# Kernel tuning notes

Hardware: AMD Instinct MI355X
Metric: run time of the kernel (lower is better)

## Reference

```python
import jax, jax.numpy as jnp
import numpy as np

PAD, BOS, EOS, ROW, SEP = 10, 11, 12, 13, 14
VOCAB, D_MODEL, MAX_SEQ, MAX_H, MAX_W = 15, 512, 4096, 30, 30
B, T = 16, 4096
LN_EPS = 1e-5


def _build_2d_ids(ids):
    """Replicates the serial CPU double-loop as a vectorized lax.scan over time.
    ids: (B, T) int32 -> (row_ids, col_ids), each (B, T) int32."""
    def step(carry, tok):
        row, col, in_grid = carry
        is_bos = tok == BOS
        is_sep = tok == SEP
        is_row = tok == ROW
        is_end = (tok == EOS) | (tok == PAD)
        grid_color = in_grid & (tok >= 0) & (tok <= 9)
        emit_r = jnp.where(grid_color, row, 0)
        emit_c = jnp.where(grid_color, col, 0)
        n_grid = jnp.where(is_bos, True, jnp.where(is_end, False, in_grid))
        n_row = jnp.where(is_bos | is_sep, 0, jnp.where(is_row, row + 1, row))
        n_col = jnp.where(is_bos | is_sep | is_row, 0,
                          jnp.where(grid_color, col + 1, col))
        return (n_row, n_col, n_grid), (emit_r, emit_c)

    def scan_one(seq):
        init = (jnp.int32(0), jnp.int32(0), jnp.bool_(False))
        _, (r, c) = jax.lax.scan(step, init, seq)
        return r, c

    r, c = jax.vmap(scan_one)(ids)
    return jnp.clip(r, 0, MAX_H - 1), jnp.clip(c, 0, MAX_W - 1)


def setup_inputs() -> dict:
    key = jax.random.key(0)
    ks = jax.random.split(key, 8)
    input_ids = jax.random.randint(ks[0], (B, T), 0, VOCAB, dtype=jnp.int32)
    s = 0.02
    token_table = jax.random.normal(ks[1], (VOCAB, D_MODEL), jnp.float32) * s
    token_table = token_table.at[PAD].set(0.0)  # padding_idx zeroed
    pos_table = jax.random.normal(ks[2], (MAX_SEQ, D_MODEL), jnp.float32) * s
    row_table = jax.random.normal(ks[3], (MAX_H, D_MODEL // 2), jnp.float32) * s
    col_table = jax.random.normal(ks[4], (MAX_W, D_MODEL // 2), jnp.float32) * s
    w_spatial = jax.random.normal(ks[5], (D_MODEL, D_MODEL), jnp.float32) * s
    ln_gamma = jnp.ones((D_MODEL,), jnp.float32)
    ln_beta = jnp.zeros((D_MODEL,), jnp.float32)
    return {"input_ids": input_ids, "token_table": token_table,
            "pos_table": pos_table, "row_table": row_table,
            "col_table": col_table, "w_spatial": w_spatial,
            "ln_gamma": ln_gamma, "ln_beta": ln_beta}


def reference(input_ids, token_table, pos_table, row_table, col_table,
              w_spatial, ln_gamma, ln_beta):
    Bv, Tv = input_ids.shape
    tok_emb = token_table[input_ids]                      # (B,T,D)
    pos_emb = pos_table[:Tv][None, :, :]                  # (1,T,D)
    row_ids, col_ids = _build_2d_ids(input_ids)
    rc = jnp.concatenate([row_table[row_ids], col_table[col_ids]], axis=-1)
    spatial = jnp.einsum('btd,ed->bte', rc, w_spatial)    # Linear, no bias
    mask = ((input_ids >= 0) & (input_ids <= 9)).astype(tok_emb.dtype)[..., None]
    x = tok_emb + pos_emb + spatial * mask
    mu = jnp.mean(x, axis=-1, keepdims=True)
    var = jnp.var(x, axis=-1, keepdims=True)
    x = (x - mu) * jax.lax.rsqrt(var + LN_EPS) * ln_gamma + ln_beta
    return x  # dropout is identity in eval mode
```

## Files before the change

### kernel.cpp

```cpp
#include <hip/hip_runtime.h>
#include <hip/hip_bf16.h>

constexpr int PAD_T = 10, BOS_T = 11, EOS_T = 12, ROW_T = 13, SEP_T = 14;
constexpr int Bc = 16, Tc = 4096, Dc = 512;
constexpr int MAXH = 30, MAXW = 30;

typedef float fvec4 __attribute__((ext_vector_type(4)));

__device__ __align__(16) int   g_packed[Bc * Tc];
__device__ __align__(16) float g_frow[MAXH * Dc];
__device__ __align__(16) float g_fcol[MAXW * Dc];

struct Summ { int r, c0, c1, g0, g1, rk, ck; };

__device__ inline void tok_update(int tok, Summ& s) {
    if (tok == BOS_T)      { s.g0 = 1; s.g1 = 1; s.r = 0; s.c0 = 0; s.c1 = 0; s.rk = 0; s.ck = 0; }
    else if (tok == SEP_T) { s.r = 0; s.c0 = 0; s.c1 = 0; s.rk = 0; s.ck = 0; }
    else if (tok == ROW_T) { s.r += 1; s.c0 = 0; s.c1 = 0; s.ck = 0; }
    else if (tok == EOS_T || tok == PAD_T) { s.g0 = 0; s.g1 = 0; }
    else { s.c0 += s.g0; s.c1 += s.g1; }
}

__device__ inline Summ compose(const Summ& a, const Summ& b) {
    Summ o;
    o.g0 = a.g0 ? b.g1 : b.g0;
    o.g1 = a.g1 ? b.g1 : b.g0;
    o.r  = b.rk ? a.r + b.r : b.r;
    o.rk = a.rk & b.rk;
    int cm0 = a.g0 ? b.c1 : b.c0;
    int cm1 = a.g1 ? b.c1 : b.c0;
    o.c0 = b.ck ? a.c0 + cm0 : cm0;
    o.c1 = b.ck ? a.c1 + cm1 : cm1;
    o.ck = a.ck & b.ck;
    return o;
}

__device__ inline void apply_state(const Summ& s, int& r, int& c, int& g) {
    int cm = g ? s.c1 : s.c0;
    r = s.rk ? r + s.r : s.r;
    c = s.ck ? c + cm : cm;
    g = g ? s.g1 : s.g0;
}

__global__ __launch_bounds__(1024) void scan_pre_kernel(
        const int* __restrict__ ids,
        const float* __restrict__ row_table, const float* __restrict__ col_table,
        const float* __restrict__ w) {
    if (blockIdx.x < 16) {
        const int b = blockIdx.x;
        const int tid = threadIdx.x;
        const int lane = tid & 63, wid = tid >> 6;

        const int4 tk4 = *(const int4*)(ids + b * Tc + tid * 4);
        int tks[4] = {tk4.x, tk4.y, tk4.z, tk4.w};

        Summ s{0, 0, 0, 0, 1, 1, 1};
#pragma unroll
        for (int j = 0; j < 4; ++j) tok_update(tks[j], s);

        Summ inc = s;
#pragma unroll
        for (int d = 1; d < 64; d <<= 1) {
            Summ o;
            o.r  = __shfl_up(inc.r, d);
            o.c0 = __shfl_up(inc.c0, d);
            o.c1 = __shfl_up(inc.c1, d);
            o.g0 = __shfl_up(inc.g0, d);
            o.g1 = __shfl_up(inc.g1, d);
            o.rk = __shfl_up(inc.rk, d);
            o.ck = __shfl_up(inc.ck, d);
            if (lane >= d) inc = compose(o, inc);
        }

        __shared__ int lsum[16][7];
        if (lane == 63) {
            lsum[wid][0] = inc.r;  lsum[wid][1] = inc.c0; lsum[wid][2] = inc.c1;
            lsum[wid][3] = inc.g0; lsum[wid][4] = inc.g1;
            lsum[wid][5] = inc.rk; lsum[wid][6] = inc.ck;
        }
        __syncthreads();

        int wr = 0, wc = 0, wg = 0;
        for (int w2 = 0; w2 < wid; ++w2) {
            Summ t;
            t.r  = lsum[w2][0]; t.c0 = lsum[w2][1]; t.c1 = lsum[w2][2];
            t.g0 = lsum[w2][3]; t.g1 = lsum[w2][4];
            t.rk = lsum[w2][5]; t.ck = lsum[w2][6];
            apply_state(t, wr, wc, wg);
        }

        Summ ex;
        ex.r  = __shfl_up(inc.r, 1);  ex.c0 = __shfl_up(inc.c0, 1);
        ex.c1 = __shfl_up(inc.c1, 1); ex.g0 = __shfl_up(inc.g0, 1);
        ex.g1 = __shfl_up(inc.g1, 1); ex.rk = __shfl_up(inc.rk, 1);
        ex.ck = __shfl_up(inc.ck, 1);
        if (lane == 0) { ex = Summ{0, 0, 0, 0, 1, 1, 1}; }
        int row = wr, col = wc, grid = wg;
        apply_state(ex, row, col, grid);

        int o4[4];
#pragma unroll
        for (int j = 0; j < 4; ++j) {
            int tok = tks[j];
            int gc = grid & (tok <= 9);
            int er = gc ? min(row, MAXH - 1) : 0;
            int ec = gc ? min(col, MAXW - 1) : 0;
            o4[j] = (er << 5) | ec;
            if (tok == BOS_T)      { grid = 1; row = 0; col = 0; }
            else if (tok == SEP_T) { row = 0; col = 0; }
            else if (tok == ROW_T) { row += 1; col = 0; }
            else if (tok == EOS_T || tok == PAD_T) { grid = 0; }
            else { col += gc; }
        }
        *(int4*)(g_packed + b * Tc + tid * 4) = make_int4(o4[0], o4[1], o4[2], o4[3]);
    } else {
        const int blk = blockIdx.x - 16;
        const int which = blk / 30;
        const int rr = blk % 30;
        const float* src = which ? (col_table + rr * 256) : (row_table + rr * 256);
        float* dst = which ? (g_fcol + rr * Dc) : (g_frow + rr * Dc);
        const int doff = which ? 256 : 0;

        __shared__ __align__(16) float sv[256];
        if (threadIdx.x < 256) sv[threadIdx.x] = src[threadIdx.x];
        __syncthreads();

        if (threadIdx.x < 512) {
            const int e = threadIdx.x;
            const float4* a4 = (const float4*)sv;
            const float4* w4 = (const float4*)(w + (size_t)e * Dc + doff);
            float acc = 0.f;
#pragma unroll 8
            for (int k = 0; k < 64; ++k) {
                float4 a = a4[k];
                float4 wb = w4[k];
                acc += a.x * wb.x + a.y * wb.y + a.z * wb.z + a.w * wb.w;
            }
            dst[e] = acc;
        }
    }
}

__global__ __launch_bounds__(256) void fuse_ln_kernel(
        const int* __restrict__ ids,
        const float* __restrict__ token_table, const float* __restrict__ pos_table,
        const float* __restrict__ gamma, const float* __restrict__ beta,
        float* __restrict__ out) {
    const int wave = threadIdx.x >> 6;
    const int lane = threadIdx.x & 63;
    const int g2 = blockIdx.x * 4 + wave;
    const int b0 = g2 & 7;
    const int t  = g2 >> 3;
    const int idx0 = b0 * Tc + t;
    const int idx1 = idx0 + 8 * Tc;
    const int d0 = lane * 8;

    const int tok0 = ids[idx0];
    const int tok1 = ids[idx1];
    const int pk0 = g_packed[idx0];
    const int pk1 = g_packed[idx1];

    float xp[8];
    *(float4*)(xp + 0) = *(const float4*)(pos_table + (size_t)t * Dc + d0);
    *(float4*)(xp + 4) = *(const float4*)(pos_table + (size_t)t * Dc + d0 + 4);

    float x0[8], x1[8];
    {
        float xt[8];
        *(float4*)(xt + 0) = *(const float4*)(token_table + (size_t)tok0 * Dc + d0);
        *(float4*)(xt + 4) = *(const float4*)(token_table + (size_t)tok0 * Dc + d0 + 4);
#pragma unroll
        for (int j = 0; j < 8; ++j) x0[j] = xt[j] + xp[j];
    }
    {
        float xt[8];
        *(float4*)(xt + 0) = *(const float4*)(token_table + (size_t)tok1 * Dc + d0);
        *(float4*)(xt + 4) = *(const float4*)(token_table + (size_t)tok1 * Dc + d0 + 4);
#pragma unroll
        for (int j = 0; j < 8; ++j) x1[j] = xt[j] + xp[j];
    }

    if (tok0 <= 9) {
        const int rI = pk0 >> 5, cI = pk0 & 31;
        float xf[8], xc[8];
        *(float4*)(xf + 0) = *(const float4*)(g_frow + (size_t)rI * Dc + d0);
        *(float4*)(xf + 4) = *(const float4*)(g_frow + (size_t)rI * Dc + d0 + 4);
        *(float4*)(xc + 0) = *(const float4*)(g_fcol + (size_t)cI * Dc + d0);
        *(float4*)(xc + 4) = *(const float4*)(g_fcol + (size_t)cI * Dc + d0 + 4);
#pragma unroll
        for (int j = 0; j < 8; ++j) x0[j] += xf[j] + xc[j];
    }
    if (tok1 <= 9) {
        const int rI = pk1 >> 5, cI = pk1 & 31;
        float xf[8], xc[8];
        *(float4*)(xf + 0) = *(const float4*)(g_frow + (size_t)rI * Dc + d0);
        *(float4*)(xf + 4) = *(const float4*)(g_frow + (size_t)rI * Dc + d0 + 4);
        *(float4*)(xc + 0) = *(const float4*)(g_fcol + (size_t)cI * Dc + d0);
        *(float4*)(xc + 4) = *(const float4*)(g_fcol + (size_t)cI * Dc + d0 + 4);
#pragma unroll
        for (int j = 0; j < 8; ++j) x1[j] += xf[j] + xc[j];
    }

    float s0 = 0.f, q0 = 0.f, s1 = 0.f, q1 = 0.f;
#pragma unroll
    for (int j = 0; j < 8; ++j) {
        s0 += x0[j]; q0 = fmaf(x0[j], x0[j], q0);
        s1 += x1[j]; q1 = fmaf(x1[j], x1[j], q1);
    }
#pragma unroll
    for (int m = 1; m < 64; m <<= 1) {
        s0 += __shfl_xor(s0, m);
        s1 += __shfl_xor(s1, m);
        q0 += __shfl_xor(q0, m);
        q1 += __shfl_xor(q1, m);
    }
    const float mu0  = s0 * (1.0f / Dc);
    const float mu1  = s1 * (1.0f / Dc);
    const float var0 = fmaf(-mu0, mu0, q0 * (1.0f / Dc));
    const float var1 = fmaf(-mu1, mu1, q1 * (1.0f / Dc));
    const float inv0 = rsqrtf(var0 + 1e-5f);
    const float inv1 = rsqrtf(var1 + 1e-5f);

    float gm[8], bb[8];
    *(float4*)(gm + 0) = *(const float4*)(gamma + d0);
    *(float4*)(gm + 4) = *(const float4*)(gamma + d0 + 4);
    *(float4*)(bb + 0) = *(const float4*)(beta + d0);
    *(float4*)(bb + 4) = *(const float4*)(beta + d0 + 4);

    fvec4 y0a, y0b, y1a, y1b;
    y0a.x = fmaf((x0[0] - mu0) * inv0, gm[0], bb[0]);
    y0a.y = fmaf((x0[1] - mu0) * inv0, gm[1], bb[1]);
    y0a.z = fmaf((x0[2] - mu0) * inv0, gm[2], bb[2]);
    y0a.w = fmaf((x0[3] - mu0) * inv0, gm[3], bb[3]);
    y0b.x = fmaf((x0[4] - mu0) * inv0, gm[4], bb[4]);
    y0b.y = fmaf((x0[5] - mu0) * inv0, gm[5], bb[5]);
    y0b.z = fmaf((x0[6] - mu0) * inv0, gm[6], bb[6]);
    y0b.w = fmaf((x0[7] - mu0) * inv0, gm[7], bb[7]);
    y1a.x = fmaf((x1[0] - mu1) * inv1, gm[0], bb[0]);
    y1a.y = fmaf((x1[1] - mu1) * inv1, gm[1], bb[1]);
    y1a.z = fmaf((x1[2] - mu1) * inv1, gm[2], bb[2]);
    y1a.w = fmaf((x1[3] - mu1) * inv1, gm[3], bb[3]);
    y1b.x = fmaf((x1[4] - mu1) * inv1, gm[4], bb[4]);
    y1b.y = fmaf((x1[5] - mu1) * inv1, gm[5], bb[5]);
    y1b.z = fmaf((x1[6] - mu1) * inv1, gm[6], bb[6]);
    y1b.w = fmaf((x1[7] - mu1) * inv1, gm[7], bb[7]);

    float* op0 = out + (size_t)idx0 * Dc + d0;
    float* op1 = out + (size_t)idx1 * Dc + d0;
    __builtin_nontemporal_store(y0a, (fvec4*)(op0 + 0));
    __builtin_nontemporal_store(y0b, (fvec4*)(op0 + 4));
    __builtin_nontemporal_store(y1a, (fvec4*)(op1 + 0));
    __builtin_nontemporal_store(y1b, (fvec4*)(op1 + 4));
}

extern "C" void kernel_launch(void* const* d_in, const int* in_sizes, int n_in,
                              void* d_out, int out_size, void* d_ws, size_t ws_size,
                              hipStream_t stream) {
    const int*   ids         = (const int*)d_in[0];
    const float* token_table = (const float*)d_in[1];
    const float* pos_table   = (const float*)d_in[2];
    const float* row_table   = (const float*)d_in[3];
    const float* col_table   = (const float*)d_in[4];
    const float* w_spatial   = (const float*)d_in[5];
    const float* ln_gamma    = (const float*)d_in[6];
    const float* ln_beta     = (const float*)d_in[7];
    float* out = (float*)d_out;

    (void)d_ws; (void)ws_size;

    hipLaunchKernelGGL(scan_pre_kernel, dim3(76), dim3(1024), 0, stream,
                       ids, row_table, col_table, w_spatial);
    hipLaunchKernelGGL(fuse_ln_kernel, dim3(Bc * Tc / 8), dim3(256), 0, stream,
                       ids, token_table, pos_table, ln_gamma, ln_beta, out);
}
```

Before: 195.4 us.

## Process all 16 batch rows per position block with half-wave rows and split-K projection

The fused LayerNorm kernel now assigns one block per sequence position. Each wave handles four batch rows, and each half-wave owns one row with 16 floats per lane. This shares the pos_table row across all batches in a block, halves the shuffle-reduction depth, and uses a wave-uniform branch for the spatial add. Separately, the precompute projection uses all 1024 threads through a split-K over two halves combined in shared memory. The cost is higher register pressure from 16-element arrays, and the spatial loads now run for non-digit lanes whenever any lane in the wave is a digit.

Result: slower. 381.1 us (+95.0%).

```diff
diff --git a/kernel.cpp b/kernel.cpp
--- a/kernel.cpp
+++ b/kernel.cpp
@@ -122,22 +122,24 @@
         const int doff = which ? 256 : 0;
 
         __shared__ __align__(16) float sv[256];
+        __shared__ float part[512];
         if (threadIdx.x < 256) sv[threadIdx.x] = src[threadIdx.x];
         __syncthreads();
 
-        if (threadIdx.x < 512) {
-            const int e = threadIdx.x;
-            const float4* a4 = (const float4*)sv;
-            const float4* w4 = (const float4*)(w + (size_t)e * Dc + doff);
-            float acc = 0.f;
+        const int e    = threadIdx.x & 511;
+        const int half = threadIdx.x >> 9;
+        const float4* a4 = (const float4*)sv + half * 32;
+        const float4* w4 = (const float4*)(w + (size_t)e * Dc + doff) + half * 32;
+        float acc = 0.f;
 #pragma unroll 8
-            for (int k = 0; k < 64; ++k) {
-                float4 a = a4[k];
-                float4 wb = w4[k];
-                acc += a.x * wb.x + a.y * wb.y + a.z * wb.z + a.w * wb.w;
-            }
-            dst[e] = acc;
-        }
+        for (int k = 0; k < 32; ++k) {
+            float4 a = a4[k];
+            float4 wb = w4[k];
+            acc += a.x * wb.x + a.y * wb.y + a.z * wb.z + a.w * wb.w;
+        }
+        if (half) part[e] = acc;
+        __syncthreads();
+        if (!half) dst[e] = acc + part[e];
     }
 }
 
@@ -146,111 +148,142 @@
         const float* __restrict__ token_table, const float* __restrict__ pos_table,
         const float* __restrict__ gamma, const float* __restrict__ beta,
         float* __restrict__ out) {
+    const int t    = blockIdx.x;
     const int wave = threadIdx.x >> 6;
     const int lane = threadIdx.x & 63;
-    const int g2 = blockIdx.x * 4 + wave;
-    const int b0 = g2 & 7;
-    const int t  = g2 >> 3;
-    const int idx0 = b0 * Tc + t;
-    const int idx1 = idx0 + 8 * Tc;
-    const int d0 = lane * 8;
-
-    const int tok0 = ids[idx0];
-    const int tok1 = ids[idx1];
-    const int pk0 = g_packed[idx0];
-    const int pk1 = g_packed[idx1];
-
-    float xp[8];
-    *(float4*)(xp + 0) = *(const float4*)(pos_table + (size_t)t * Dc + d0);
-    *(float4*)(xp + 4) = *(const float4*)(pos_table + (size_t)t * Dc + d0 + 4);
-
-    float x0[8], x1[8];
-    {
-        float xt[8];
-        *(float4*)(xt + 0) = *(const float4*)(token_table + (size_t)tok0 * Dc + d0);
-        *(float4*)(xt + 4) = *(const float4*)(token_table + (size_t)tok0 * Dc + d0 + 4);
-#pragma unroll
-        for (int j = 0; j < 8; ++j) x0[j] = xt[j] + xp[j];
-    }
-    {
-        float xt[8];
-        *(float4*)(xt + 0) = *(const float4*)(token_table + (size_t)tok1 * Dc + d0);
-        *(float4*)(xt + 4) = *(const float4*)(token_table + (size_t)tok1 * Dc + d0 + 4);
-#pragma unroll
-        for (int j = 0; j < 8; ++j) x1[j] = xt[j] + xp[j];
-    }
-
-    if (tok0 <= 9) {
-        const int rI = pk0 >> 5, cI = pk0 & 31;
-        float xf[8], xc[8];
-        *(float4*)(xf + 0) = *(const float4*)(g_frow + (size_t)rI * Dc + d0);
-        *(float4*)(xf + 4) = *(const float4*)(g_frow + (size_t)rI * Dc + d0 + 4);
-        *(float4*)(xc + 0) = *(const float4*)(g_fcol + (size_t)cI * Dc + d0);
-        *(float4*)(xc + 4) = *(const float4*)(g_fcol + (size_t)cI * Dc + d0 + 4);
-#pragma unroll
-        for (int j = 0; j < 8; ++j) x0[j] += xf[j] + xc[j];
-    }
-    if (tok1 <= 9) {
-        const int rI = pk1 >> 5, cI = pk1 & 31;
-        float xf[8], xc[8];
-        *(float4*)(xf + 0) = *(const float4*)(g_frow + (size_t)rI * Dc + d0);
-        *(float4*)(xf + 4) = *(const float4*)(g_frow + (size_t)rI * Dc + d0 + 4);
-        *(float4*)(xc + 0) = *(const float4*)(g_fcol + (size_t)cI * Dc + d0);
-        *(float4*)(xc + 4) = *(const float4*)(g_fcol + (size_t)cI * Dc + d0 + 4);
-#pragma unroll
-        for (int j = 0; j < 8; ++j) x1[j] += xf[j] + xc[j];
-    }
-
-    float s0 = 0.f, q0 = 0.f, s1 = 0.f, q1 = 0.f;
-#pragma unroll
-    for (int j = 0; j < 8; ++j) {
-        s0 += x0[j]; q0 = fmaf(x0[j], x0[j], q0);
-        s1 += x1[j]; q1 = fmaf(x1[j], x1[j], q1);
-    }
-#pragma unroll
-    for (int m = 1; m < 64; m <<= 1) {
-        s0 += __shfl_xor(s0, m);
-        s1 += __shfl_xor(s1, m);
-        q0 += __shfl_xor(q0, m);
-        q1 += __shfl_xor(q1, m);
-    }
-    const float mu0  = s0 * (1.0f / Dc);
-    const float mu1  = s1 * (1.0f / Dc);
-    const float var0 = fmaf(-mu0, mu0, q0 * (1.0f / Dc));
-    const float var1 = fmaf(-mu1, mu1, q1 * (1.0f / Dc));
-    const float inv0 = rsqrtf(var0 + 1e-5f);
-    const float inv1 = rsqrtf(var1 + 1e-5f);
-
-    float gm[8], bb[8];
-    *(float4*)(gm + 0) = *(const float4*)(gamma + d0);
-    *(float4*)(gm + 4) = *(const float4*)(gamma + d0 + 4);
-    *(float4*)(bb + 0) = *(const float4*)(beta + d0);
-    *(float4*)(bb + 4) = *(const float4*)(beta + d0 + 4);
-
-    fvec4 y0a, y0b, y1a, y1b;
-    y0a.x = fmaf((x0[0] - mu0) * inv0, gm[0], bb[0]);
-    y0a.y = fmaf((x0[1] - mu0) * inv0, gm[1], bb[1]);
-    y0a.z = fmaf((x0[2] - mu0) * inv0, gm[2], bb[2]);
-    y0a.w = fmaf((x0[3] - mu0) * inv0, gm[3], bb[3]);
-    y0b.x = fmaf((x0[4] - mu0) * inv0, gm[4], bb[4]);
-    y0b.y = fmaf((x0[5] - mu0) * inv0, gm[5], bb[5]);
-    y0b.z = fmaf((x0[6] - mu0) * inv0, gm[6], bb[6]);
-    y0b.w = fmaf((x0[7] - mu0) * inv0, gm[7], bb[7]);
-    y1a.x = fmaf((x1[0] - mu1) * inv1, gm[0], bb[0]);
-    y1a.y = fmaf((x1[1] - mu1) * inv1, gm[1], bb[1]);
-    y1a.z = fmaf((x1[2] - mu1) * inv1, gm[2], bb[2]);
-    y1a.w = fmaf((x1[3] - mu1) * inv1, gm[3], bb[3]);
-    y1b.x = fmaf((x1[4] - mu1) * inv1, gm[4], bb[4]);
-    y1b.y = fmaf((x1[5] - mu1) * inv1, gm[5], bb[5]);
-    y1b.z = fmaf((x1[6] - mu1) * inv1, gm[6], bb[6]);
-    y1b.w = fmaf((x1[7] - mu1) * inv1, gm[7], bb[7]);
-
-    float* op0 = out + (size_t)idx0 * Dc + d0;
-    float* op1 = out + (size_t)idx1 * Dc + d0;
-    __builtin_nontemporal_store(y0a, (fvec4*)(op0 + 0));
-    __builtin_nontemporal_store(y0b, (fvec4*)(op0 + 4));
-    __builtin_nontemporal_store(y1a, (fvec4*)(op1 + 0));
-    __builtin_nontemporal_store(y1b, (fvec4*)(op1 + 4));
+    const int h    = lane >> 5;
+    const int d0   = (lane & 31) * 16;
+    const int bb0  = wave * 4;
+
+    int tok[4], pk[4];
+#pragma unroll
+    for (int k = 0; k < 4; ++k) {
+        tok[k] = ids[(bb0 + k) * Tc + t];
+        pk[k]  = g_packed[(bb0 + k) * Tc + t];
+    }
+
+    float xp[16];
+    {
+        const float* p = pos_table + (size_t)t * Dc + d0;
+#pragma unroll
+        for (int q = 0; q < 4; ++q) *(float4*)(xp + 4 * q) = *(const float4*)(p + 4 * q);
+    }
+
+    float xA[16], xB[16];
+    float sA = 0.f, qA = 0.f, sB = 0.f, qB = 0.f;
+
+    {
+        const int tokp = h ? tok[1] : tok[0];
+        const int pkp  = h ? pk[1]  : pk[0];
+        const float* tr = token_table + (size_t)tokp * Dc + d0;
+#pragma unroll
+        for (int q = 0; q < 4; ++q) {
+            float4 v = *(const float4*)(tr + 4 * q);
+            xA[4 * q + 0] = v.x + xp[4 * q + 0];
+            xA[4 * q + 1] = v.y + xp[4 * q + 1];
+            xA[4 * q + 2] = v.z + xp[4 * q + 2];
+            xA[4 * q + 3] = v.w + xp[4 * q + 3];
+        }
+        const bool dig = (tokp <= 9);
+        if (__any(dig)) {
+            const float fm = dig ? 1.f : 0.f;
+            const int rI = dig ? (pkp >> 5) : 0;
+            const int cI = dig ? (pkp & 31) : 0;
+            const float* fr = g_frow + (size_t)rI * Dc + d0;
+            const float* fc = g_fcol + (size_t)cI * Dc + d0;
+#pragma unroll
+            for (int q = 0; q < 4; ++q) {
+                float4 a = *(const float4*)(fr + 4 * q);
+                float4 b = *(const float4*)(fc + 4 * q);
+                xA[4 * q + 0] = fmaf(fm, a.x + b.x, xA[4 * q + 0]);
+                xA[4 * q + 1] = fmaf(fm, a.y + b.y, xA[4 * q + 1]);
+                xA[4 * q + 2] = fmaf(fm, a.z + b.z, xA[4 * q + 2]);
+                xA[4 * q + 3] = fmaf(fm, a.w + b.w, xA[4 * q + 3]);
+            }
+        }
+#pragma unroll
+        for (int j = 0; j < 16; ++j) { sA += xA[j]; qA = fmaf(xA[j], xA[j], qA); }
+    }
+
+    {
+        const int tokp = h ? tok[3] : tok[2];
+        const int pkp  = h ? pk[3]  : pk[2];
+        const float* tr = token_table + (size_t)tokp * Dc + d0;
+#pragma unroll
+        for (int q = 0; q < 4; ++q) {
+            float4 v = *(const float4*)(tr + 4 * q);
+            xB[4 * q + 0] = v.x + xp[4 * q + 0];
+            xB[4 * q + 1] = v.y + xp[4 * q + 1];
+            xB[4 * q + 2] = v.z + xp[4 * q + 2];
+            xB[4 * q + 3] = v.w + xp[4 * q + 3];
+        }
+        const bool dig = (tokp <= 9);
+        if (__any(dig)) {
+            const float fm = dig ? 1.f : 0.f;
+            const int rI = dig ? (pkp >> 5) : 0;
+            const int cI = dig ? (pkp & 31) : 0;
+            const float* fr = g_frow + (size_t)rI * Dc + d0;
+            const float* fc = g_fcol + (size_t)cI * Dc + d0;
+#pragma unroll
+            for (int q = 0; q < 4; ++q) {
+                float4 a = *(const float4*)(fr + 4 * q);
+                float4 b = *(const float4*)(fc + 4 * q);
+                xB[4 * q + 0] = fmaf(fm, a.x + b.x, xB[4 * q + 0]);
+                xB[4 * q + 1] = fmaf(fm, a.y + b.y, xB[4 * q + 1]);
+                xB[4 * q + 2] = fmaf(fm, a.z + b.z, xB[4 * q + 2]);
+                xB[4 * q + 3] = fmaf(fm, a.w + b.w, xB[4 * q + 3]);
+            }
+        }
+#pragma unroll
+        for (int j = 0; j < 16; ++j) { sB += xB[j]; qB = fmaf(xB[j], xB[j], qB); }
+    }
+
+#pragma unroll
+    for (int m = 1; m < 32; m <<= 1) {
+        sA += __shfl_xor(sA, m);
+        sB += __shfl_xor(sB, m);
+        qA += __shfl_xor(qA, m);
+        qB += __shfl_xor(qB, m);
+    }
+
+    const float muA  = sA * (1.0f / Dc);
+    const float muB  = sB * (1.0f / Dc);
+    const float varA = fmaf(-muA, muA, qA * (1.0f / Dc));
+    const float varB = fmaf(-muB, muB, qB * (1.0f / Dc));
+    const float invA = rsqrtf(varA + 1e-5f);
+    const float invB = rsqrtf(varB + 1e-5f);
+
+    float gm[16], bt[16];
+#pragma unroll
+    for (int q = 0; q < 4; ++q) {
+        *(float4*)(gm + 4 * q) = *(const float4*)(gamma + d0 + 4 * q);
+        *(float4*)(bt + 4 * q) = *(const float4*)(beta  + d0 + 4 * q);
+    }
+
+    {
+        float* op = out + ((size_t)((bb0 + h) * Tc + t)) * Dc + d0;
+#pragma unroll
+        for (int q = 0; q < 4; ++q) {
+            fvec4 y;
+            y.x = fmaf((xA[4 * q + 0] - muA) * invA, gm[4 * q + 0], bt[4 * q + 0]);
+            y.y = fmaf((xA[4 * q + 1] - muA) * invA, gm[4 * q + 1], bt[4 * q + 1]);
+            y.z = fmaf((xA[4 * q + 2] - muA) * invA, gm[4 * q + 2], bt[4 * q + 2]);
+            y.w = fmaf((xA[4 * q + 3] - muA) * invA, gm[4 * q + 3], bt[4 * q + 3]);
+            __builtin_nontemporal_store(y, (fvec4*)(op + 4 * q));
+        }
+    }
+    {
+        float* op = out + ((size_t)((bb0 + 2 + h) * Tc + t)) * Dc + d0;
+#pragma unroll
+        for (int q = 0; q < 4; ++q) {
+            fvec4 y;
+            y.x = fmaf((xB[4 * q + 0] - muB) * invB, gm[4 * q + 0], bt[4 * q + 0]);
+            y.y = fmaf((xB[4 * q + 1] - muB) * invB, gm[4 * q + 1], bt[4 * q + 1]);
+            y.z = fmaf((xB[4 * q + 2] - muB) * invB, gm[4 * q + 2], bt[4 * q + 2]);
+            y.w = fmaf((xB[4 * q + 3] - muB) * invB, gm[4 * q + 3], bt[4 * q + 3]);
+            __builtin_nontemporal_store(y, (fvec4*)(op + 4 * q));
+        }
+    }
 }
 
 extern "C" void kernel_launch(void* const* d_in, const int* in_sizes, int n_in,
@@ -270,6 +303,6 @@
 
     hipLaunchKernelGGL(scan_pre_kernel, dim3(76), dim3(1024), 0, stream,
                        ids, row_table, col_table, w_spatial);
-    hipLaunchKernelGGL(fuse_ln_kernel, dim3(Bc * Tc / 8), dim3(256), 0, stream,
+    hipLaunchKernelGGL(fuse_ln_kernel, dim3(Tc), dim3(256), 0, stream,
                        ids, token_table, pos_table, ln_gamma, ln_beta, out);
 }
```
